# Performance work log

Hardware: AMD Instinct MI355X
Metric: run time of the kernel (lower is better)

Reference implementation:

```python
import jax, jax.numpy as jnp
import numpy as np

N = 100000   # nodes
E = 1600000  # edges (before self-loops)
IN, HID, OUT = 128, 16, 10
NEG_SLOPE = 0.2
LN_EPS = 1e-5


def layer_norm(x, gamma, beta):
    mu = jnp.mean(x, axis=-1, keepdims=True)
    var = jnp.mean((x - mu) ** 2, axis=-1, keepdims=True)
    return (x - mu) * jax.lax.rsqrt(var + LN_EPS) * gamma + beta


def gat_conv(x, edge_index, W, a_src, a_dst, bias, concat):
    # x: [N, Din], W: [Din, H*F], a_src/a_dst: [H, F]
    n = x.shape[0]
    H, F = a_src.shape
    h = (x @ W).reshape(n, H, F)                      # [N, H, F]
    src, dst = edge_index[0], edge_index[1]
    alpha_src = jnp.sum(h * a_src, axis=-1)           # [N, H]
    alpha_dst = jnp.sum(h * a_dst, axis=-1)           # [N, H]
    e = jax.nn.leaky_relu(alpha_src[src] + alpha_dst[dst], NEG_SLOPE)  # [E, H]
    # segment softmax over incoming edges of each dst node (self-loops guarantee non-empty)
    m = jax.ops.segment_max(e, dst, num_segments=n)
    e = jnp.exp(e - m[dst])
    s = jax.ops.segment_sum(e, dst, num_segments=n)
    alpha = e / (s[dst] + 1e-16)                      # [E, H]
    out = jax.ops.segment_sum(h[src] * alpha[:, :, None], dst, num_segments=n)  # [N, H, F]
    out = out.reshape(n, H * F) if concat else out.mean(axis=1)
    return out + bias


def setup_inputs() -> dict:
    key = jax.random.key(0)
    ks = jax.random.split(key, 20)
    d = {}
    d["x"] = jax.random.normal(ks[0], (N, IN), dtype=jnp.float32)
    d["edge_index"] = jax.random.randint(ks[1], (2, E), 0, N, dtype=jnp.int64)
    s = 0.1
    # layer 1: IN -> HID, 8 heads, concat
    d["W1"] = jax.random.normal(ks[2], (IN, 8 * HID), jnp.float32) * s
    d["a_src1"] = jax.random.normal(ks[3], (8, HID), jnp.float32) * s
    d["a_dst1"] = jax.random.normal(ks[4], (8, HID), jnp.float32) * s
    d["b1"] = jnp.zeros((8 * HID,), jnp.float32)
    d["g1"] = jnp.ones((8 * HID,), jnp.float32)
    d["be1"] = jnp.zeros((8 * HID,), jnp.float32)
    # layer 2: 8*HID -> HID, 4 heads, concat
    d["W2"] = jax.random.normal(ks[5], (8 * HID, 4 * HID), jnp.float32) * s
    d["a_src2"] = jax.random.normal(ks[6], (4, HID), jnp.float32) * s
    d["a_dst2"] = jax.random.normal(ks[7], (4, HID), jnp.float32) * s
    d["b2"] = jnp.zeros((4 * HID,), jnp.float32)
    d["g2"] = jnp.ones((4 * HID,), jnp.float32)
    d["be2"] = jnp.zeros((4 * HID,), jnp.float32)
    # layer 3: 4*HID -> OUT, 1 head, no concat
    d["W3"] = jax.random.normal(ks[8], (4 * HID, OUT), jnp.float32) * s
    d["a_src3"] = jax.random.normal(ks[9], (1, OUT), jnp.float32) * s
    d["a_dst3"] = jax.random.normal(ks[10], (1, OUT), jnp.float32) * s
    d["b3"] = jnp.zeros((OUT,), jnp.float32)
    return d


def reference(x, edge_index, W1, a_src1, a_dst1, b1, g1, be1,
              W2, a_src2, a_dst2, b2, g2, be2,
              W3, a_src3, a_dst3, b3):
    n = x.shape[0]
    loops = jnp.arange(n, dtype=edge_index.dtype)
    ei = jnp.concatenate([edge_index, jnp.stack([loops, loops])], axis=1)  # add self-loops
    h = gat_conv(x, ei, W1, a_src1, a_dst1, b1, concat=True)
    h = jax.nn.elu(layer_norm(h, g1, be1))
    h = gat_conv(h, ei, W2, a_src2, a_dst2, b2, concat=True)
    h = jax.nn.elu(layer_norm(h, g2, be2))
    h = gat_conv(h, ei, W3, a_src3, a_dst3, b3, concat=False)
    return jax.nn.log_softmax(h, axis=1)
```

## Files before the change

### kernel.cpp

```cpp
#include <hip/hip_runtime.h>
#include <hip/hip_bf16.h>
#include <math.h>

typedef __hip_bfloat16 bf16;
typedef __bf16 bf16x8 __attribute__((ext_vector_type(8)));
typedef float floatx4 __attribute__((ext_vector_type(4)));

__device__ __forceinline__ unsigned short f2bu(float f) {
    bf16 b = __float2bfloat16(f);
    return __builtin_bit_cast(unsigned short, b);
}
__device__ __forceinline__ float bu2f(unsigned short u) {
    return __uint_as_float(((unsigned)u) << 16);
}

template<typename XT, int H>
__global__ __launch_bounds__(256) void gemm_mfma(
    const XT* __restrict__ X, const float* __restrict__ W,
    const float* __restrict__ a_src, const float* __restrict__ a_dst,
    bf16* __restrict__ Hout, float* __restrict__ asrc, float* __restrict__ adst,
    int N)
{
    constexpr int M = H * 16;
    constexpr int KP = 136;
    constexpr int NT = M / 16;
    constexpr int HPQ = H / 4;
    __shared__ __align__(16) unsigned short Wt[M * KP];
    __shared__ __align__(16) unsigned short As[64 * KP];
    __shared__ float As_s[M], Ad_s[M];
    int tid = threadIdx.x;
    int r0 = blockIdx.x * 64;

    for (int i = tid; i < M; i += 256) { As_s[i] = a_src[i]; Ad_s[i] = a_dst[i]; }
    for (int idx = tid; idx < 128 * M; idx += 256) {
        int k = idx / M, m = idx % M;
        Wt[m * KP + k] = f2bu(W[idx]);
    }
    if constexpr (__is_same(XT, float)) {
        for (int idx = tid; idx < 64 * 32; idx += 256) {
            int row = idx >> 5, c4 = (idx & 31) * 4;
            int grow = r0 + row;
            float4 v = make_float4(0.f, 0.f, 0.f, 0.f);
            if (grow < N)
                v = *reinterpret_cast<const float4*>(X + (size_t)grow * 128 + c4);
            unsigned short* a = &As[row * KP + c4];
            a[0] = f2bu(v.x); a[1] = f2bu(v.y); a[2] = f2bu(v.z); a[3] = f2bu(v.w);
        }
    } else {
        for (int idx = tid; idx < 64 * 16; idx += 256) {
            int row = idx >> 4, c8 = (idx & 15) * 8;
            int grow = r0 + row;
            uint4 v = make_uint4(0u, 0u, 0u, 0u);
            if (grow < N)
                v = *reinterpret_cast<const uint4*>((const unsigned short*)X + (size_t)grow * 128 + c8);
            *reinterpret_cast<uint4*>(&As[row * KP + c8]) = v;
        }
    }
    __syncthreads();

    int w = tid >> 6, l = tid & 63, q = l >> 4, c = l & 15;
    floatx4 acc[NT];
    #pragma unroll
    for (int t = 0; t < NT; ++t) acc[t] = (floatx4){0.f, 0.f, 0.f, 0.f};

    #pragma unroll
    for (int kc = 0; kc < 4; ++kc) {
        bf16x8 a = *reinterpret_cast<const bf16x8*>(&As[(w * 16 + c) * KP + kc * 32 + q * 8]);
        #pragma unroll
        for (int t = 0; t < NT; ++t) {
            bf16x8 b = *reinterpret_cast<const bf16x8*>(&Wt[(t * 16 + c) * KP + kc * 32 + q * 8]);
            acc[t] = __builtin_amdgcn_mfma_f32_16x16x32_bf16(a, b, acc[t], 0, 0, 0);
        }
    }
    __syncthreads();
    #pragma unroll
    for (int t = 0; t < NT; ++t)
        #pragma unroll
        for (int r = 0; r < 4; ++r)
            As[(w * 16 + q * 4 + r) * KP + t * 16 + c] = f2bu(acc[t][r]);
    __syncthreads();
    for (int idx = tid; idx < 64 * (M / 8); idx += 256) {
        int row = idx / (M / 8), g = idx % (M / 8);
        int grow = r0 + row;
        if (grow < N)
            *reinterpret_cast<uint4*>(Hout + (size_t)grow * M + g * 8) =
                *reinterpret_cast<const uint4*>(&As[row * KP + g * 8]);
    }
    {
        int r = tid >> 2, qq = tid & 3;
        int grow = r0 + r;
        if (grow < N) {
            #pragma unroll
            for (int hh = 0; hh < HPQ; ++hh) {
                int hd = qq * HPQ + hh;
                float s1 = 0.f, s2 = 0.f;
                #pragma unroll
                for (int f = 0; f < 16; f += 2) {
                    unsigned u = *reinterpret_cast<const unsigned*>(&As[r * KP + hd * 16 + f]);
                    float v0 = __uint_as_float(u << 16);
                    float v1 = __uint_as_float(u & 0xffff0000u);
                    s1 += v0 * As_s[hd * 16 + f] + v1 * As_s[hd * 16 + f + 1];
                    s2 += v0 * Ad_s[hd * 16 + f] + v1 * Ad_s[hd * 16 + f + 1];
                }
                asrc[(size_t)grow * H + hd] = s1;
                adst[(size_t)grow * H + hd] = s2;
            }
        }
    }
}

#define CSR_CH  4096
#define CSR_REG 8192

__global__ __launch_bounds__(256) void csr_hist(
    const int* __restrict__ ei, int E, int DPB, int* __restrict__ histM)
{
    __shared__ int cnt[256];
    int tid = threadIdx.x;
    cnt[tid] = 0;
    __syncthreads();
    int e0 = blockIdx.x * CSR_CH;
    int e1 = min(E, e0 + CSR_CH);
    for (int e = e0 + tid; e < e1; e += 256)
        atomicAdd(&cnt[ei[E + e] / DPB], 1);
    __syncthreads();
    histM[blockIdx.x * 256 + tid] = cnt[tid];
}

__global__ __launch_bounds__(256) void csr_colscan(
    const int* __restrict__ histM, int NBLK,
    int* __restrict__ offT, int* __restrict__ btot)
{
    __shared__ int sm[512];
    int b = blockIdx.x;
    int tid = threadIdx.x;
    int i0 = tid, i1 = tid + 256;
    sm[i0] = (i0 < NBLK) ? histM[i0 * 256 + b] : 0;
    sm[i1] = (i1 < NBLK) ? histM[i1 * 256 + b] : 0;
    __syncthreads();
    #pragma unroll
    for (int o = 1; o < 512; o <<= 1) {
        int t0 = (i0 >= o) ? sm[i0 - o] : 0;
        int t1 = (i1 >= o) ? sm[i1 - o] : 0;
        __syncthreads();
        sm[i0] += t0; sm[i1] += t1;
        __syncthreads();
    }
    if (i0 < NBLK) offT[b * NBLK + i0] = b * CSR_REG + ((i0 == 0) ? 0 : sm[i0 - 1]);
    if (i1 < NBLK) offT[b * NBLK + i1] = b * CSR_REG + sm[i1 - 1];
    if (tid == 0) btot[b] = sm[511];
}

__global__ __launch_bounds__(256) void csr_pair_scatter(
    const int* __restrict__ ei, int E, int DPB,
    const int* __restrict__ offT, int NBLK,
    unsigned* __restrict__ pairs)
{
    __shared__ int cnt[256];
    int tid = threadIdx.x;
    int blk = blockIdx.x;
    cnt[tid] = offT[tid * NBLK + blk];
    __syncthreads();
    int e0 = blk * CSR_CH;
    int e1 = min(E, e0 + CSR_CH);
    for (int e = e0 + tid; e < e1; e += 256) {
        int s = ei[e];
        int d = ei[E + e];
        int b = d / DPB;
        int dloc = d - b * DPB;
        int pos = atomicAdd(&cnt[b], 1);
        pairs[pos] = ((unsigned)dloc << 17) | (unsigned)s;
    }
}

__global__ __launch_bounds__(256) void csr_fine(
    const unsigned* __restrict__ pairs, const int* __restrict__ btot,
    int DPB, int N, int2* __restrict__ ptrSE, int* __restrict__ col)
{
    __shared__ int sm[512];
    __shared__ int off[512];
    int b = blockIdx.x;
    int tid = threadIdx.x;
    int base = b * CSR_REG;
    int tot = btot[b];
    int d0 = b * DPB;
    int i0 = tid, i1 = tid + 256;
    sm[i0] = 0; sm[i1] = 0;
    __syncthreads();
    for (int i = tid; i < tot; i += 256)
        atomicAdd(&sm[pairs[base + i] >> 17], 1);
    __syncthreads();
    #pragma unroll
    for (int o = 1; o < 512; o <<= 1) {
        int t0 = (i0 >= o) ? sm[i0 - o] : 0;
        int t1 = (i1 >= o) ? sm[i1 - o] : 0;
        __syncthreads();
        sm[i0] += t0; sm[i1] += t1;
        __syncthreads();
    }
    int s0e = base + ((i0 == 0) ? 0 : sm[i0 - 1]);
    int s1e = base + sm[i1 - 1];
    off[i0] = s0e;
    off[i1] = s1e;
    if (i0 < DPB && d0 + i0 < N) ptrSE[d0 + i0] = make_int2(s0e, base + sm[i0]);
    if (i1 < DPB && d0 + i1 < N) ptrSE[d0 + i1] = make_int2(s1e, base + sm[i1]);
    __syncthreads();
    for (int i = tid; i < tot; i += 256) {
        unsigned p = pairs[base + i];
        int pos = atomicAdd(&off[p >> 17], 1);
        col[pos] = (int)(p & 0x1FFFFu);
    }
}

template<int H, int F, int LPD>
__global__ __launch_bounds__(64) void agg_ln_kernel(
    const int2* __restrict__ ptrSE, const int* __restrict__ col,
    const float* __restrict__ asrc, const float* __restrict__ adst,
    const bf16* __restrict__ hb, const float* __restrict__ bias,
    const float* __restrict__ g, const float* __restrict__ be,
    bf16* __restrict__ out, int N)
{
    constexpr int M = H * F;
    constexpr int PF = M / LPD;
    static_assert(PF == 2, "PF must be 2");
    constexpr int DPW = 64 / LPD;
    int sub = threadIdx.x / LPD;
    int j = threadIdx.x % LPD;
    int d = blockIdx.x * DPW + sub;
    if (d >= N) return;
    int f0 = j * 2;
    int hd = f0 / F;
    int2 se = ptrSE[d];
    int e = se.x, end = se.y;
    float adst_h = adst[d * H + hd];
    const unsigned* hw = (const unsigned*)hb;

    float a00, a01, a10 = 0.f, a11 = 0.f, a20 = 0.f, a21 = 0.f, a30 = 0.f, a31 = 0.f;
    float dn0, dn1 = 0.f, dn2 = 0.f, dn3 = 0.f;

    {
        float lg = asrc[d * H + hd] + adst_h;
        lg = lg > 0.f ? lg : 0.2f * lg;
        float w = __expf(lg);
        unsigned u = hw[(size_t)d * (M / 2) + j];
        a00 = w * __uint_as_float(u << 16);
        a01 = w * __uint_as_float(u & 0xffff0000u);
        dn0 = w;
    }

    for (; e < end && (e & 3); ++e) {
        int s = col[e];
        float lg = asrc[s * H + hd] + adst_h;
        lg = lg > 0.f ? lg : 0.2f * lg;
        float w = __expf(lg);
        unsigned u = hw[(size_t)s * (M / 2) + j];
        a00 += w * __uint_as_float(u << 16);
        a01 += w * __uint_as_float(u & 0xffff0000u);
        dn0 += w;
    }
    for (; e + 4 <= end; e += 4) {
        int4 c4 = *reinterpret_cast<const int4*>(&col[e]);
        float l0 = asrc[c4.x * H + hd];
        float l1 = asrc[c4.y * H + hd];
        float l2 = asrc[c4.z * H + hd];
        float l3 = asrc[c4.w * H + hd];
        unsigned u0 = hw[(size_t)c4.x * (M / 2) + j];
        unsigned u1 = hw[(size_t)c4.y * (M / 2) + j];
        unsigned u2 = hw[(size_t)c4.z * (M / 2) + j];
        unsigned u3 = hw[(size_t)c4.w * (M / 2) + j];
        l0 += adst_h; l0 = l0 > 0.f ? l0 : 0.2f * l0; float w0 = __expf(l0);
        l1 += adst_h; l1 = l1 > 0.f ? l1 : 0.2f * l1; float w1 = __expf(l1);
        l2 += adst_h; l2 = l2 > 0.f ? l2 : 0.2f * l2; float w2 = __expf(l2);
        l3 += adst_h; l3 = l3 > 0.f ? l3 : 0.2f * l3; float w3 = __expf(l3);
        a00 += w0 * __uint_as_float(u0 << 16);
        a01 += w0 * __uint_as_float(u0 & 0xffff0000u);
        a10 += w1 * __uint_as_float(u1 << 16);
        a11 += w1 * __uint_as_float(u1 & 0xffff0000u);
        a20 += w2 * __uint_as_float(u2 << 16);
        a21 += w2 * __uint_as_float(u2 & 0xffff0000u);
        a30 += w3 * __uint_as_float(u3 << 16);
        a31 += w3 * __uint_as_float(u3 & 0xffff0000u);
        dn0 += w0; dn1 += w1; dn2 += w2; dn3 += w3;
    }
    for (; e < end; ++e) {
        int s = col[e];
        float lg = asrc[s * H + hd] + adst_h;
        lg = lg > 0.f ? lg : 0.2f * lg;
        float w = __expf(lg);
        unsigned u = hw[(size_t)s * (M / 2) + j];
        a00 += w * __uint_as_float(u << 16);
        a01 += w * __uint_as_float(u & 0xffff0000u);
        dn0 += w;
    }

    float den = dn0 + dn1 + dn2 + dn3;
    float rden = 1.f / (den + 1e-16f);
    float o0 = (a00 + a10 + a20 + a30) * rden + bias[f0];
    float o1 = (a01 + a11 + a21 + a31) * rden + bias[f0 + 1];
    float sm1 = o0 + o1, sm2 = o0 * o0 + o1 * o1;
    #pragma unroll
    for (int off = LPD / 2; off >= 1; off >>= 1) {
        sm1 += __shfl_xor(sm1, off, LPD);
        sm2 += __shfl_xor(sm2, off, LPD);
    }
    float mu = sm1 * (1.f / M);
    float var = sm2 * (1.f / M) - mu * mu;
    float inv = rsqrtf(var + 1e-5f);
    float y0 = (o0 - mu) * inv * g[f0] + be[f0];
    float y1 = (o1 - mu) * inv * g[f0 + 1] + be[f0 + 1];
    y0 = y0 > 0.f ? y0 : expm1f(y0);
    y1 = y1 > 0.f ? y1 : expm1f(y1);
    unsigned u = (unsigned)f2bu(y0) | ((unsigned)f2bu(y1) << 16);
    *reinterpret_cast<unsigned*>((unsigned short*)out + (size_t)d * M + f0) = u;
}

__global__ __launch_bounds__(256) void gemm3_alpha(
    const bf16* __restrict__ X, const float* __restrict__ W3,
    const float* __restrict__ av_src, const float* __restrict__ av_dst,
    bf16* __restrict__ h3, float* __restrict__ asrc, float* __restrict__ adst,
    int N)
{
    __shared__ float Wl[640];
    int tid = threadIdx.x;
    for (int i = tid; i < 640; i += 256) Wl[i] = W3[i];
    __syncthreads();
    int n = blockIdx.x * 256 + tid;
    if (n >= N) return;
    float h[10];
    #pragma unroll
    for (int j = 0; j < 10; ++j) h[j] = 0.f;
    const unsigned short* xr = (const unsigned short*)X + (size_t)n * 64;
    for (int k2 = 0; k2 < 32; ++k2) {
        unsigned u = *reinterpret_cast<const unsigned*>(xr + k2 * 2);
        float x0 = __uint_as_float(u << 16);
        float x1 = __uint_as_float(u & 0xffff0000u);
        #pragma unroll
        for (int j = 0; j < 10; ++j)
            h[j] += x0 * Wl[(k2 * 2) * 10 + j] + x1 * Wl[(k2 * 2 + 1) * 10 + j];
    }
    float s1 = 0.f, s2 = 0.f;
    unsigned short* hr = (unsigned short*)h3 + (size_t)n * 16;
    #pragma unroll
    for (int j = 0; j < 10; j += 2) {
        unsigned u = (unsigned)f2bu(h[j]) | ((unsigned)f2bu(h[j + 1]) << 16);
        *reinterpret_cast<unsigned*>(hr + j) = u;
    }
    #pragma unroll
    for (int j = 0; j < 10; ++j) {
        s1 += h[j] * av_src[j];
        s2 += h[j] * av_dst[j];
    }
    asrc[n] = s1;
    adst[n] = s2;
}

__global__ __launch_bounds__(256) void agg_l3_final(
    const int2* __restrict__ ptrSE, const int* __restrict__ col,
    const float* __restrict__ asrc, const float* __restrict__ adst,
    const bf16* __restrict__ h, const float* __restrict__ b3,
    float* __restrict__ out, int N)
{
    int tid = threadIdx.x;
    int sub16 = tid >> 4;
    int j = tid & 15;
    int d = blockIdx.x * 16 + sub16;
    if (d >= N) return;
    const unsigned short* hu = (const unsigned short*)h;
    int2 se = ptrSE[d];
    int e = se.x, end = se.y;
    float adst_d = adst[d];
    float lg = asrc[d] + adst_d;
    lg = lg > 0.f ? lg : 0.2f * lg;
    float w = __expf(lg);
    bool act = j < 10;
    float a0 = act ? w * bu2f(hu[(size_t)d * 16 + j]) : 0.f;
    float a1 = 0.f, a2 = 0.f, a3 = 0.f;
    float d0 = w, d1 = 0.f, d2 = 0.f, d3 = 0.f;
    for (; e + 4 <= end; e += 4) {
        int s0 = col[e + 0], s1 = col[e + 1], s2 = col[e + 2], s3 = col[e + 3];
        float l0 = asrc[s0], l1 = asrc[s1], l2 = asrc[s2], l3 = asrc[s3];
        float v0 = act ? bu2f(hu[(size_t)s0 * 16 + j]) : 0.f;
        float v1 = act ? bu2f(hu[(size_t)s1 * 16 + j]) : 0.f;
        float v2 = act ? bu2f(hu[(size_t)s2 * 16 + j]) : 0.f;
        float v3 = act ? bu2f(hu[(size_t)s3 * 16 + j]) : 0.f;
        l0 += adst_d; l0 = l0 > 0.f ? l0 : 0.2f * l0; float w0 = __expf(l0);
        l1 += adst_d; l1 = l1 > 0.f ? l1 : 0.2f * l1; float w1 = __expf(l1);
        l2 += adst_d; l2 = l2 > 0.f ? l2 : 0.2f * l2; float w2 = __expf(l2);
        l3 += adst_d; l3 = l3 > 0.f ? l3 : 0.2f * l3; float w3 = __expf(l3);
        a0 += w0 * v0; a1 += w1 * v1; a2 += w2 * v2; a3 += w3 * v3;
        d0 += w0; d1 += w1; d2 += w2; d3 += w3;
    }
    for (; e < end; ++e) {
        int s = col[e];
        float l = asrc[s] + adst_d;
        l = l > 0.f ? l : 0.2f * l;
        float ww = __expf(l);
        if (act) a0 += ww * bu2f(hu[(size_t)s * 16 + j]);
        d0 += ww;
    }
    float den = d0 + d1 + d2 + d3;
    float v = (a0 + a1 + a2 + a3) / (den + 1e-16f);
    float lv = act ? v + b3[j] : -1e30f;
    float mx = lv;
    #pragma unroll
    for (int off = 1; off < 16; off <<= 1) mx = fmaxf(mx, __shfl_xor(mx, off, 16));
    float ev = act ? __expf(lv - mx) : 0.f;
    float se2 = ev;
    #pragma unroll
    for (int off = 1; off < 16; off <<= 1) se2 += __shfl_xor(se2, off, 16);
    float ls = mx + logf(se2);
    if (act) out[(size_t)d * 10 + j] = lv - ls;
}

static inline int cdiv(long a, long b) { return (int)((a + b - 1) / b); }

extern "C" void kernel_launch(void* const* d_in, const int* in_sizes, int n_in,
                              void* d_out, int out_size, void* d_ws, size_t ws_size,
                              hipStream_t stream)
{
    const float* x   = (const float*)d_in[0];
    const int*   ei  = (const int*)d_in[1];
    const float* W1  = (const float*)d_in[2];
    const float* as1 = (const float*)d_in[3];
    const float* ad1 = (const float*)d_in[4];
    const float* b1  = (const float*)d_in[5];
    const float* g1  = (const float*)d_in[6];
    const float* be1 = (const float*)d_in[7];
    const float* W2  = (const float*)d_in[8];
    const float* as2 = (const float*)d_in[9];
    const float* ad2 = (const float*)d_in[10];
    const float* b2  = (const float*)d_in[11];
    const float* g2  = (const float*)d_in[12];
    const float* be2 = (const float*)d_in[13];
    const float* W3  = (const float*)d_in[14];
    const float* as3 = (const float*)d_in[15];
    const float* ad3 = (const float*)d_in[16];
    const float* b3  = (const float*)d_in[17];

    const int N = in_sizes[0] / 128;
    const int E = in_sizes[1] / 2;

    const int DPB  = cdiv(N, 256);
    const int NBLK = cdiv(E, CSR_CH);

    bf16*     hb    = (bf16*)d_ws;
    bf16*     aggb  = hb + (size_t)N * 128;
    float*    asrc  = (float*)(aggb + (size_t)N * 128);
    float*    adst  = asrc + (size_t)N * 8;
    unsigned* pairs = (unsigned*)(adst + (size_t)N * 8);
    int*      col   = (int*)(pairs + 256 * CSR_REG);
    int2*     ptrSE = (int2*)(col + 256 * CSR_REG);
    int*      histM = (int*)(ptrSE + N);
    int*      offT  = histM + (size_t)NBLK * 256;
    int*      btot  = offT + (size_t)NBLK * 256;
    bf16*     h3b   = hb;

    csr_hist<<<NBLK, 256, 0, stream>>>(ei, E, DPB, histM);
    csr_colscan<<<256, 256, 0, stream>>>(histM, NBLK, offT, btot);
    csr_pair_scatter<<<NBLK, 256, 0, stream>>>(ei, E, DPB, offT, NBLK, pairs);
    csr_fine<<<256, 256, 0, stream>>>(pairs, btot, DPB, N, ptrSE, col);

    gemm_mfma<float, 8><<<cdiv(N, 64), 256, 0, stream>>>(x, W1, as1, ad1, hb, asrc, adst, N);
    agg_ln_kernel<8, 16, 64><<<N, 64, 0, stream>>>(ptrSE, col, asrc, adst, hb, b1, g1, be1, aggb, N);

    gemm_mfma<bf16, 4><<<cdiv(N, 64), 256, 0, stream>>>(aggb, W2, as2, ad2, hb, asrc, adst, N);
    agg_ln_kernel<4, 16, 32><<<cdiv(N, 2), 64, 0, stream>>>(ptrSE, col, asrc, adst, hb, b2, g2, be2, aggb, N);

    gemm3_alpha<<<cdiv(N, 256), 256, 0, stream>>>(aggb, W3, as3, ad3, h3b, asrc, adst, N);
    agg_l3_final<<<cdiv(N, 16), 256, 0, stream>>>(ptrSE, col, asrc, adst, h3b, b3, (float*)d_out, N);
}
```

Measured before the change: 405.4 us.

## Widen per-lane features in GAT aggregation kernels with vector bf16 loads

The aggregation+LayerNorm kernel now gives each lane several features (8 for layer 1, 4 for layer 2) loaded as 128-bit or 64-bit bf16 vectors, instead of 2 features per lane across 64 or 32 lanes. Each wave now processes 4 destination nodes in layer 1 and 4 in layer 2, in 256-thread blocks. This cuts the number of lanes that redundantly compute the same attention weight per edge and issues fewer, wider gathers. The trade-off is that the 4-way edge unroll becomes 2-way, so fewer independent loads are in flight per lane, and load imbalance between nodes in the same wave may grow.

```diff
diff --git a/kernel.cpp b/kernel.cpp
--- a/kernel.cpp
+++ b/kernel.cpp
@@ -12,6 +12,24 @@
 }
 __device__ __forceinline__ float bu2f(unsigned short u) {
     return __uint_as_float(((unsigned)u) << 16);
+}
+
+template<int PF>
+__device__ __forceinline__ void ldbfv(const unsigned short* p, float* v) {
+    if constexpr (PF == 8) {
+        uint4 u = *reinterpret_cast<const uint4*>(p);
+        v[0] = __uint_as_float(u.x << 16); v[1] = __uint_as_float(u.x & 0xffff0000u);
+        v[2] = __uint_as_float(u.y << 16); v[3] = __uint_as_float(u.y & 0xffff0000u);
+        v[4] = __uint_as_float(u.z << 16); v[5] = __uint_as_float(u.z & 0xffff0000u);
+        v[6] = __uint_as_float(u.w << 16); v[7] = __uint_as_float(u.w & 0xffff0000u);
+    } else if constexpr (PF == 4) {
+        uint2 u = *reinterpret_cast<const uint2*>(p);
+        v[0] = __uint_as_float(u.x << 16); v[1] = __uint_as_float(u.x & 0xffff0000u);
+        v[2] = __uint_as_float(u.y << 16); v[3] = __uint_as_float(u.y & 0xffff0000u);
+    } else {
+        unsigned u = *reinterpret_cast<const unsigned*>(p);
+        v[0] = __uint_as_float(u << 16); v[1] = __uint_as_float(u & 0xffff0000u);
+    }
 }
 
 template<typename XT, int H>
@@ -212,92 +230,78 @@
     }
 }
 
-template<int H, int F, int LPD>
-__global__ __launch_bounds__(64) void agg_ln_kernel(
+template<int M, int LPD>
+__global__ __launch_bounds__(256) void agg_ln_kernel(
     const int2* __restrict__ ptrSE, const int* __restrict__ col,
     const float* __restrict__ asrc, const float* __restrict__ adst,
     const bf16* __restrict__ hb, const float* __restrict__ bias,
     const float* __restrict__ g, const float* __restrict__ be,
     bf16* __restrict__ out, int N)
 {
-    constexpr int M = H * F;
     constexpr int PF = M / LPD;
-    static_assert(PF == 2, "PF must be 2");
-    constexpr int DPW = 64 / LPD;
-    int sub = threadIdx.x / LPD;
-    int j = threadIdx.x % LPD;
-    int d = blockIdx.x * DPW + sub;
+    constexpr int H = M / 16;
+    constexpr int DPBk = 256 / LPD;
+    int tid = threadIdx.x;
+    int sub = tid / LPD;
+    int j = tid % LPD;
+    int d = blockIdx.x * DPBk + sub;
     if (d >= N) return;
-    int f0 = j * 2;
-    int hd = f0 / F;
+    int f0 = j * PF;
+    int hd = f0 / 16;
     int2 se = ptrSE[d];
     int e = se.x, end = se.y;
     float adst_h = adst[d * H + hd];
-    const unsigned* hw = (const unsigned*)hb;
-
-    float a00, a01, a10 = 0.f, a11 = 0.f, a20 = 0.f, a21 = 0.f, a30 = 0.f, a31 = 0.f;
-    float dn0, dn1 = 0.f, dn2 = 0.f, dn3 = 0.f;
-
+    const unsigned short* hw = (const unsigned short*)hb;
+
+    float ac0[PF], ac1[PF];
+    float dn0, dn1 = 0.f;
     {
         float lg = asrc[d * H + hd] + adst_h;
         lg = lg > 0.f ? lg : 0.2f * lg;
         float w = __expf(lg);
-        unsigned u = hw[(size_t)d * (M / 2) + j];
-        a00 = w * __uint_as_float(u << 16);
-        a01 = w * __uint_as_float(u & 0xffff0000u);
+        float v[PF];
+        ldbfv<PF>(hw + (size_t)d * M + f0, v);
+        #pragma unroll
+        for (int p = 0; p < PF; ++p) { ac0[p] = w * v[p]; ac1[p] = 0.f; }
         dn0 = w;
     }
-
-    for (; e < end && (e & 3); ++e) {
-        int s = col[e];
-        float lg = asrc[s * H + hd] + adst_h;
-        lg = lg > 0.f ? lg : 0.2f * lg;
-        float w = __expf(lg);
-        unsigned u = hw[(size_t)s * (M / 2) + j];
-        a00 += w * __uint_as_float(u << 16);
-        a01 += w * __uint_as_float(u & 0xffff0000u);
-        dn0 += w;
-    }
-    for (; e + 4 <= end; e += 4) {
-        int4 c4 = *reinterpret_cast<const int4*>(&col[e]);
-        float l0 = asrc[c4.x * H + hd];
-        float l1 = asrc[c4.y * H + hd];
-        float l2 = asrc[c4.z * H + hd];
-        float l3 = asrc[c4.w * H + hd];
-        unsigned u0 = hw[(size_t)c4.x * (M / 2) + j];
-        unsigned u1 = hw[(size_t)c4.y * (M / 2) + j];
-        unsigned u2 = hw[(size_t)c4.z * (M / 2) + j];
-        unsigned u3 = hw[(size_t)c4.w * (M / 2) + j];
+    for (; e + 2 <= end; e += 2) {
+        int s0 = col[e], s1 = col[e + 1];
+        float l0 = asrc[s0 * H + hd];
+        float l1 = asrc[s1 * H + hd];
+        float v0[PF], v1[PF];
+        ldbfv<PF>(hw + (size_t)s0 * M + f0, v0);
+        ldbfv<PF>(hw + (size_t)s1 * M + f0, v1);
         l0 += adst_h; l0 = l0 > 0.f ? l0 : 0.2f * l0; float w0 = __expf(l0);
         l1 += adst_h; l1 = l1 > 0.f ? l1 : 0.2f * l1; float w1 = __expf(l1);
-        l2 += adst_h; l2 = l2 > 0.f ? l2 : 0.2f * l2; float w2 = __expf(l2);
-        l3 += adst_h; l3 = l3 > 0.f ? l3 : 0.2f * l3; float w3 = __expf(l3);
-        a00 += w0 * __uint_as_float(u0 << 16);
-        a01 += w0 * __uint_as_float(u0 & 0xffff0000u);
-        a10 += w1 * __uint_as_float(u1 << 16);
-        a11 += w1 * __uint_as_float(u1 & 0xffff0000u);
-        a20 += w2 * __uint_as_float(u2 << 16);
-        a21 += w2 * __uint_as_float(u2 & 0xffff0000u);
-        a30 += w3 * __uint_as_float(u3 << 16);
-        a31 += w3 * __uint_as_float(u3 & 0xffff0000u);
-        dn0 += w0; dn1 += w1; dn2 += w2; dn3 += w3;
+        #pragma unroll
+        for (int p = 0; p < PF; ++p) {
+            ac0[p] += w0 * v0[p];
+            ac1[p] += w1 * v1[p];
+        }
+        dn0 += w0; dn1 += w1;
     }
     for (; e < end; ++e) {
         int s = col[e];
         float lg = asrc[s * H + hd] + adst_h;
         lg = lg > 0.f ? lg : 0.2f * lg;
         float w = __expf(lg);
-        unsigned u = hw[(size_t)s * (M / 2) + j];
-        a00 += w * __uint_as_float(u << 16);
-        a01 += w * __uint_as_float(u & 0xffff0000u);
+        float v[PF];
+        ldbfv<PF>(hw + (size_t)s * M + f0, v);
+        #pragma unroll
+        for (int p = 0; p < PF; ++p) ac0[p] += w * v[p];
         dn0 += w;
     }
 
-    float den = dn0 + dn1 + dn2 + dn3;
-    float rden = 1.f / (den + 1e-16f);
-    float o0 = (a00 + a10 + a20 + a30) * rden + bias[f0];
-    float o1 = (a01 + a11 + a21 + a31) * rden + bias[f0 + 1];
-    float sm1 = o0 + o1, sm2 = o0 * o0 + o1 * o1;
+    float rden = 1.f / (dn0 + dn1 + 1e-16f);
+    float o[PF];
+    float sm1 = 0.f, sm2 = 0.f;
+    #pragma unroll
+    for (int p = 0; p < PF; ++p) {
+        o[p] = (ac0[p] + ac1[p]) * rden + bias[f0 + p];
+        sm1 += o[p];
+        sm2 += o[p] * o[p];
+    }
     #pragma unroll
     for (int off = LPD / 2; off >= 1; off >>= 1) {
         sm1 += __shfl_xor(sm1, off, LPD);
@@ -306,12 +310,22 @@
     float mu = sm1 * (1.f / M);
     float var = sm2 * (1.f / M) - mu * mu;
     float inv = rsqrtf(var + 1e-5f);
-    float y0 = (o0 - mu) * inv * g[f0] + be[f0];
-    float y1 = (o1 - mu) * inv * g[f0 + 1] + be[f0 + 1];
-    y0 = y0 > 0.f ? y0 : expm1f(y0);
-    y1 = y1 > 0.f ? y1 : expm1f(y1);
-    unsigned u = (unsigned)f2bu(y0) | ((unsigned)f2bu(y1) << 16);
-    *reinterpret_cast<unsigned*>((unsigned short*)out + (size_t)d * M + f0) = u;
+    unsigned pk[PF / 2];
+    #pragma unroll
+    for (int p = 0; p < PF; p += 2) {
+        float y0 = (o[p] - mu) * inv * g[f0 + p] + be[f0 + p];
+        float y1 = (o[p + 1] - mu) * inv * g[f0 + p + 1] + be[f0 + p + 1];
+        y0 = y0 > 0.f ? y0 : expm1f(y0);
+        y1 = y1 > 0.f ? y1 : expm1f(y1);
+        pk[p / 2] = (unsigned)f2bu(y0) | ((unsigned)f2bu(y1) << 16);
+    }
+    unsigned short* op = (unsigned short*)out + (size_t)d * M + f0;
+    if constexpr (PF == 8)
+        *reinterpret_cast<uint4*>(op) = make_uint4(pk[0], pk[1], pk[2], pk[3]);
+    else if constexpr (PF == 4)
+        *reinterpret_cast<uint2*>(op) = make_uint2(pk[0], pk[1]);
+    else
+        *reinterpret_cast<unsigned*>(op) = pk[0];
 }
 
 __global__ __launch_bounds__(256) void gemm3_alpha(
@@ -461,10 +475,10 @@
     csr_fine<<<256, 256, 0, stream>>>(pairs, btot, DPB, N, ptrSE, col);
 
     gemm_mfma<float, 8><<<cdiv(N, 64), 256, 0, stream>>>(x, W1, as1, ad1, hb, asrc, adst, N);
-    agg_ln_kernel<8, 16, 64><<<N, 64, 0, stream>>>(ptrSE, col, asrc, adst, hb, b1, g1, be1, aggb, N);
+    agg_ln_kernel<128, 16><<<cdiv(N, 16), 256, 0, stream>>>(ptrSE, col, asrc, adst, hb, b1, g1, be1, aggb, N);
 
     gemm_mfma<bf16, 4><<<cdiv(N, 64), 256, 0, stream>>>(aggb, W2, as2, ad2, hb, asrc, adst, N);
-    agg_ln_kernel<4, 16, 32><<<cdiv(N, 2), 64, 0, stream>>>(ptrSE, col, asrc, adst, hb, b2, g2, be2, aggb, N);
+    agg_ln_kernel<64, 16><<<cdiv(N, 16), 256, 0, stream>>>(ptrSE, col, asrc, adst, hb, b2, g2, be2, aggb, N);
 
     gemm3_alpha<<<cdiv(N, 256), 256, 0, stream>>>(aggb, W3, as3, ad3, h3b, asrc, adst, N);
     agg_l3_final<<<cdiv(N, 16), 256, 0, stream>>>(ptrSE, col, asrc, adst, h3b, b3, (float*)d_out, N);
```

New measurement: 388.6 us. -4.1%, faster.
